# Optimization experiments

Measured on AMD Instinct MI355X. Metric: run time of the kernel, lower is better.

Reference implementation:

```python
import jax, jax.numpy as jnp
import numpy as np

BATCH, TIME, IN, HID = 32, 512, 512, 1024
THRESHOLD = 1.0
BETA = 1.0 / 2.0  # 1/tau


def setup_inputs() -> dict:
    key = jax.random.key(0)
    kx, kw, kb = jax.random.split(key, 3)
    x = jax.random.normal(kx, (BATCH, TIME, IN), dtype=jnp.float32)
    bound = 1.0 / np.sqrt(IN)  # nn.Linear default init range
    W = jax.random.uniform(kw, (HID, IN), minval=-bound, maxval=bound, dtype=jnp.float32)
    b = jax.random.uniform(kb, (HID,), minval=-bound, maxval=bound, dtype=jnp.float32)
    return {"x": x, "W": W, "b": b}


def reference(x, W, b):
    # Precompute all per-step linear projections in one big GEMM: [B,T,H]
    hidden = jnp.einsum("bti,hi->bth", x, W) + b

    def step(mem, h_t):
        # h_t: [B,H]
        mem = BETA * mem + h_t
        spk = (mem > THRESHOLD).astype(h_t.dtype)
        mem = mem * (1.0 - spk)  # hard reset
        return mem, spk

    mem0 = jnp.zeros((x.shape[0], W.shape[0]), dtype=x.dtype)
    # scan over time: [T,B,H]
    _, spikes = jax.lax.scan(step, mem0, jnp.swapaxes(hidden, 0, 1))
    return jnp.swapaxes(spikes, 0, 1)  # [B,T,H]
```

## Files before the change

### kernel.cpp

```cpp
#include <hip/hip_runtime.h>

#define BATCH 32
#define TIME  512
#define INF   512
#define HIDF  1024

#define MBT  128
#define NBH  128
#define KCH  16
#define NCH  (INF / KCH)
#define TILEF (MBT * KCH)

#define GLD16(g, l) __builtin_amdgcn_global_load_lds(                      \
    (const __attribute__((address_space(1))) void*)(g),                    \
    (__attribute__((address_space(3))) void*)(l), 16, 0, 0)

__global__ __launch_bounds__(256, 3)
void snn_gemm_seqfma(const float* __restrict__ x, const float* __restrict__ W,
                     const float* __restrict__ bias, float* __restrict__ hidden) {
    __shared__ __align__(16) float xs[2 * TILEF];
    __shared__ __align__(16) float ws[2 * TILEF];

    const int tid = threadIdx.x;
    const int l   = tid & 63;
    const int wv  = __builtin_amdgcn_readfirstlane(tid >> 6);
    const int lx  = l & 7;
    const int ly  = (l >> 3) & 7;
    const int bt0 = blockIdx.y * MBT;
    const int h0  = blockIdx.x * NBH;
    const int wbt = 64 * (wv >> 1);
    const int wh  = 64 * (wv & 1);

    const int rl   = l >> 2;
    const int qs   = (l & 3) ^ ((rl >> 1) & 3);
    const int rowA = 32 * wv + rl;
    const int rowB = rowA + 16;
    const float* xgA = x + (size_t)(bt0 + rowA) * INF + qs * 4;
    const float* xgB = x + (size_t)(bt0 + rowB) * INF + qs * 4;
    const float* wgA = W + (size_t)(h0 + rowA) * INF + qs * 4;
    const float* wgB = W + (size_t)(h0 + rowB) * INF + qs * 4;
    const int dOffA = (32 * wv) * KCH;
    const int dOffB = dOffA + 16 * KCH;

    GLD16(xgA, xs + dOffA);
    GLD16(xgB, xs + dOffB);
    GLD16(wgA, ws + dOffA);
    GLD16(wgB, ws + dOffB);

    float acc[8][8];
    #pragma unroll
    for (int r = 0; r < 8; ++r)
        #pragma unroll
        for (int c = 0; c < 8; ++c) acc[r][c] = 0.0f;

    const int keyx = (ly >> 1) & 3;
    const int keyw = (lx >> 1) & 3;

    __syncthreads();

    for (int kc = 0; kc < NCH; ++kc) {
        const int p  = kc & 1;
        const int np = p ^ 1;

        if (kc + 1 < NCH) {
            const int so = (kc + 1) * KCH;
            float* xd = xs + np * TILEF;
            float* wd = ws + np * TILEF;
            GLD16(xgA + so, xd + dOffA);
            GLD16(xgB + so, xd + dOffB);
            GLD16(wgA + so, wd + dOffA);
            GLD16(wgB + so, wd + dOffB);
        }

        const float* xrow = xs + p * TILEF + (wbt + ly) * KCH;
        const float* wrow = ws + p * TILEF + (wh  + lx) * KCH;
        #pragma unroll
        for (int g = 0; g < 4; ++g) {
            const float* xg_ = xrow + (g ^ keyx) * 4;
            const float* wg_ = wrow + (g ^ keyw) * 4;
            float4 xf[8], wf[8];
            #pragma unroll
            for (int r = 0; r < 8; ++r)
                xf[r] = *(const float4*)(xg_ + r * 8 * KCH);
            #pragma unroll
            for (int c = 0; c < 8; ++c)
                wf[c] = *(const float4*)(wg_ + c * 8 * KCH);
            #pragma unroll
            for (int r = 0; r < 8; ++r)
                #pragma unroll
                for (int c = 0; c < 8; ++c)
                    acc[r][c] = __fmaf_rn(xf[r].x, wf[c].x, acc[r][c]);
            #pragma unroll
            for (int r = 0; r < 8; ++r)
                #pragma unroll
                for (int c = 0; c < 8; ++c)
                    acc[r][c] = __fmaf_rn(xf[r].y, wf[c].y, acc[r][c]);
            #pragma unroll
            for (int r = 0; r < 8; ++r)
                #pragma unroll
                for (int c = 0; c < 8; ++c)
                    acc[r][c] = __fmaf_rn(xf[r].z, wf[c].z, acc[r][c]);
            #pragma unroll
            for (int r = 0; r < 8; ++r)
                #pragma unroll
                for (int c = 0; c < 8; ++c)
                    acc[r][c] = __fmaf_rn(xf[r].w, wf[c].w, acc[r][c]);
        }
        __syncthreads();
    }

    float bv[8];
    #pragma unroll
    for (int c = 0; c < 8; ++c) bv[c] = bias[h0 + wh + lx + 8 * c];
    #pragma unroll
    for (int r = 0; r < 8; ++r) {
        float* orow = hidden + (size_t)(bt0 + wbt + ly + 8 * r) * HIDF
                             + h0 + wh + lx;
        #pragma unroll
        for (int c = 0; c < 8; ++c)
            orow[8 * c] = __fadd_rn(acc[r][c], bv[c]);
    }
}

__global__ __launch_bounds__(64)
void snn_scan_np(float* __restrict__ io) {
    const int n = blockIdx.x * 64 + threadIdx.x;
    const int b = n >> 10;
    const int h = n & 1023;
    float* p = io + (size_t)b * TIME * HIDF + h;

    float mem = 0.0f;
    for (int tb = 0; tb < TIME / 64; ++tb) {
        float hv[64];
        #pragma unroll
        for (int u = 0; u < 64; ++u) hv[u] = p[(size_t)(tb * 64 + u) * HIDF];
        float sp[64];
        #pragma unroll
        for (int u = 0; u < 64; ++u) {
            mem = __fadd_rn(__fmul_rn(0.5f, mem), hv[u]);
            bool s = mem > 1.0f;
            sp[u] = s ? 1.0f : 0.0f;
            if (s) mem = 0.0f;
        }
        #pragma unroll
        for (int u = 0; u < 64; ++u) p[(size_t)(tb * 64 + u) * HIDF] = sp[u];
    }
}

extern "C" void kernel_launch(void* const* d_in, const int* in_sizes, int n_in,
                              void* d_out, int out_size, void* d_ws, size_t ws_size,
                              hipStream_t stream) {
    const float* x    = (const float*)d_in[0];
    const float* W    = (const float*)d_in[1];
    const float* bias = (const float*)d_in[2];
    float* out = (float*)d_out;

    dim3 g1(HIDF / NBH, (BATCH * TIME) / MBT);
    snn_gemm_seqfma<<<g1, 256, 0, stream>>>(x, W, bias, out);

    snn_scan_np<<<(BATCH * HIDF) / 64, 64, 0, stream>>>(out);
}
```

Baseline: 327.9 us.

## Enlarge GEMM M-tile to 256 with 16x8 per-thread tile; vectorize scan to float2

The GEMM block tile grows from 128x128 to 256x128, so each thread accumulates a 16x8 register tile and reuses each W fragment across twice as many rows. The X fragment is now loaded per row inside the inner loop rather than all up front, and occupancy drops to 2 blocks per SM. The scan kernel now has each thread handle two adjacent hidden units using float2 loads and stores, halving the thread count and widening memory accesses. The larger register tile raises register pressure and may cause spills or lower occupancy.

```diff
diff --git a/kernel.cpp b/kernel.cpp
--- a/kernel.cpp
+++ b/kernel.cpp
@@ -5,21 +5,22 @@
 #define INF   512
 #define HIDF  1024
 
-#define MBT  128
+#define MBT  256
 #define NBH  128
 #define KCH  16
 #define NCH  (INF / KCH)
-#define TILEF (MBT * KCH)
+#define XTILEF (MBT * KCH)
+#define WTILEF (NBH * KCH)
 
 #define GLD16(g, l) __builtin_amdgcn_global_load_lds(                      \
     (const __attribute__((address_space(1))) void*)(g),                    \
     (__attribute__((address_space(3))) void*)(l), 16, 0, 0)
 
-__global__ __launch_bounds__(256, 3)
+__global__ __launch_bounds__(256, 2)
 void snn_gemm_seqfma(const float* __restrict__ x, const float* __restrict__ W,
                      const float* __restrict__ bias, float* __restrict__ hidden) {
-    __shared__ __align__(16) float xs[2 * TILEF];
-    __shared__ __align__(16) float ws[2 * TILEF];
+    __shared__ __align__(16) float xs[2 * XTILEF];
+    __shared__ __align__(16) float ws[2 * WTILEF];
 
     const int tid = threadIdx.x;
     const int l   = tid & 63;
@@ -28,28 +29,26 @@
     const int ly  = (l >> 3) & 7;
     const int bt0 = blockIdx.y * MBT;
     const int h0  = blockIdx.x * NBH;
-    const int wbt = 64 * (wv >> 1);
+    const int wbt = 128 * (wv >> 1);
     const int wh  = 64 * (wv & 1);
 
-    const int rl   = l >> 2;
-    const int qs   = (l & 3) ^ ((rl >> 1) & 3);
-    const int rowA = 32 * wv + rl;
-    const int rowB = rowA + 16;
-    const float* xgA = x + (size_t)(bt0 + rowA) * INF + qs * 4;
-    const float* xgB = x + (size_t)(bt0 + rowB) * INF + qs * 4;
-    const float* wgA = W + (size_t)(h0 + rowA) * INF + qs * 4;
-    const float* wgB = W + (size_t)(h0 + rowB) * INF + qs * 4;
-    const int dOffA = (32 * wv) * KCH;
-    const int dOffB = dOffA + 16 * KCH;
+    const int rl = l >> 2;
+    const int qs = (l & 3) ^ ((rl >> 1) & 3);
+    const float* xg0 = x + (size_t)(bt0 + 64 * wv + rl) * INF + qs * 4;
+    const float* wg0 = W + (size_t)(h0 + 32 * wv + rl) * INF + qs * 4;
+    const int xOff = (64 * wv) * KCH;
+    const int wOff = (32 * wv) * KCH;
 
-    GLD16(xgA, xs + dOffA);
-    GLD16(xgB, xs + dOffB);
-    GLD16(wgA, ws + dOffA);
-    GLD16(wgB, ws + dOffB);
+    GLD16(xg0,            xs + xOff);
+    GLD16(xg0 + 16 * INF, xs + xOff + 256);
+    GLD16(xg0 + 32 * INF, xs + xOff + 512);
+    GLD16(xg0 + 48 * INF, xs + xOff + 768);
+    GLD16(wg0,            ws + wOff);
+    GLD16(wg0 + 16 * INF, ws + wOff + 256);
 
-    float acc[8][8];
+    float acc[16][8];
     #pragma unroll
-    for (int r = 0; r < 8; ++r)
+    for (int r = 0; r < 16; ++r)
         #pragma unroll
         for (int c = 0; c < 8; ++c) acc[r][c] = 0.0f;
 
@@ -64,47 +63,42 @@
 
         if (kc + 1 < NCH) {
             const int so = (kc + 1) * KCH;
-            float* xd = xs + np * TILEF;
-            float* wd = ws + np * TILEF;
-            GLD16(xgA + so, xd + dOffA);
-            GLD16(xgB + so, xd + dOffB);
-            GLD16(wgA + so, wd + dOffA);
-            GLD16(wgB + so, wd + dOffB);
+            float* xd = xs + np * XTILEF;
+            float* wd = ws + np * WTILEF;
+            GLD16(xg0 + so,            xd + xOff);
+            GLD16(xg0 + so + 16 * INF, xd + xOff + 256);
+            GLD16(xg0 + so + 32 * INF, xd + xOff + 512);
+            GLD16(xg0 + so + 48 * INF, xd + xOff + 768);
+            GLD16(wg0 + so,            wd + wOff);
+            GLD16(wg0 + so + 16 * INF, wd + wOff + 256);
         }
 
-        const float* xrow = xs + p * TILEF + (wbt + ly) * KCH;
-        const float* wrow = ws + p * TILEF + (wh  + lx) * KCH;
+        const float* xrow = xs + p * XTILEF + (wbt + ly) * KCH;
+        const float* wrow = ws + p * WTILEF + (wh  + lx) * KCH;
         #pragma unroll
         for (int g = 0; g < 4; ++g) {
             const float* xg_ = xrow + (g ^ keyx) * 4;
             const float* wg_ = wrow + (g ^ keyw) * 4;
-            float4 xf[8], wf[8];
-            #pragma unroll
-            for (int r = 0; r < 8; ++r)
-                xf[r] = *(const float4*)(xg_ + r * 8 * KCH);
+            float4 wf[8];
             #pragma unroll
             for (int c = 0; c < 8; ++c)
                 wf[c] = *(const float4*)(wg_ + c * 8 * KCH);
             #pragma unroll
-            for (int r = 0; r < 8; ++r)
+            for (int r = 0; r < 16; ++r) {
+                float4 xf = *(const float4*)(xg_ + r * 8 * KCH);
                 #pragma unroll
                 for (int c = 0; c < 8; ++c)
-                    acc[r][c] = __fmaf_rn(xf[r].x, wf[c].x, acc[r][c]);
-            #pragma unroll
-            for (int r = 0; r < 8; ++r)
+                    acc[r][c] = __fmaf_rn(xf.x, wf[c].x, acc[r][c]);
                 #pragma unroll
                 for (int c = 0; c < 8; ++c)
-                    acc[r][c] = __fmaf_rn(xf[r].y, wf[c].y, acc[r][c]);
-            #pragma unroll
-            for (int r = 0; r < 8; ++r)
+                    acc[r][c] = __fmaf_rn(xf.y, wf[c].y, acc[r][c]);
                 #pragma unroll
                 for (int c = 0; c < 8; ++c)
-                    acc[r][c] = __fmaf_rn(xf[r].z, wf[c].z, acc[r][c]);
-            #pragma unroll
-            for (int r = 0; r < 8; ++r)
+                    acc[r][c] = __fmaf_rn(xf.z, wf[c].z, acc[r][c]);
                 #pragma unroll
                 for (int c = 0; c < 8; ++c)
-                    acc[r][c] = __fmaf_rn(xf[r].w, wf[c].w, acc[r][c]);
+                    acc[r][c] = __fmaf_rn(xf.w, wf[c].w, acc[r][c]);
+            }
         }
         __syncthreads();
     }
@@ -113,7 +107,7 @@
     #pragma unroll
     for (int c = 0; c < 8; ++c) bv[c] = bias[h0 + wh + lx + 8 * c];
     #pragma unroll
-    for (int r = 0; r < 8; ++r) {
+    for (int r = 0; r < 16; ++r) {
         float* orow = hidden + (size_t)(bt0 + wbt + ly + 8 * r) * HIDF
                              + h0 + wh + lx;
         #pragma unroll
@@ -124,26 +118,28 @@
 
 __global__ __launch_bounds__(64)
 void snn_scan_np(float* __restrict__ io) {
-    const int n = blockIdx.x * 64 + threadIdx.x;
-    const int b = n >> 10;
-    const int h = n & 1023;
-    float* p = io + (size_t)b * TIME * HIDF + h;
+    const int n  = blockIdx.x * 64 + threadIdx.x;
+    const int b  = n >> 9;
+    const int h2 = n & 511;
+    float2* p = (float2*)io + (size_t)b * TIME * 512 + h2;
 
-    float mem = 0.0f;
-    for (int tb = 0; tb < TIME / 64; ++tb) {
-        float hv[64];
+    float m0 = 0.0f, m1 = 0.0f;
+    for (int tb = 0; tb < TIME / 32; ++tb) {
+        float2 v[32];
         #pragma unroll
-        for (int u = 0; u < 64; ++u) hv[u] = p[(size_t)(tb * 64 + u) * HIDF];
-        float sp[64];
+        for (int u = 0; u < 32; ++u) v[u] = p[(size_t)(tb * 32 + u) * 512];
         #pragma unroll
-        for (int u = 0; u < 64; ++u) {
-            mem = __fadd_rn(__fmul_rn(0.5f, mem), hv[u]);
-            bool s = mem > 1.0f;
-            sp[u] = s ? 1.0f : 0.0f;
-            if (s) mem = 0.0f;
+        for (int u = 0; u < 32; ++u) {
+            m0 = __fadd_rn(__fmul_rn(0.5f, m0), v[u].x);
+            m1 = __fadd_rn(__fmul_rn(0.5f, m1), v[u].y);
+            bool s0 = m0 > 1.0f, s1 = m1 > 1.0f;
+            v[u].x = s0 ? 1.0f : 0.0f;
+            v[u].y = s1 ? 1.0f : 0.0f;
+            if (s0) m0 = 0.0f;
+            if (s1) m1 = 0.0f;
         }
         #pragma unroll
-        for (int u = 0; u < 64; ++u) p[(size_t)(tb * 64 + u) * HIDF] = sp[u];
+        for (int u = 0; u < 32; ++u) p[(size_t)(tb * 32 + u) * 512] = v[u];
     }
 }
 
@@ -158,5 +154,5 @@
     dim3 g1(HIDF / NBH, (BATCH * TIME) / MBT);
     snn_gemm_seqfma<<<g1, 256, 0, stream>>>(x, W, bias, out);
 
-    snn_scan_np<<<(BATCH * HIDF) / 64, 64, 0, stream>>>(out);
+    snn_scan_np<<<(BATCH * HIDF / 2) / 64, 64, 0, stream>>>(out);
 }
```

New measurement: 335.1 us. 1.02x slower.
